# Kernel optimization log

Hardware: AMD Instinct MI355X
Metric: run time of the kernel (lower is better)

## Reference

```python
import jax, jax.numpy as jnp
import numpy as np

B, D, U = 8192, 2048, 2048  # batch rows, input dim, units
NB_FACTOR = 3
MASK_DENSITY = 1.0 / 16.0  # butterfly-like sparse factor density


def _glorot_uniform(key, shape):
    fan_in, fan_out = shape[0], shape[-1]
    limit = np.sqrt(6.0 / (fan_in + fan_out)).astype(np.float32)
    return jax.random.uniform(key, shape, jnp.float32, -limit, limit)


def setup_inputs() -> dict:
    key = jax.random.key(0)
    kx, km0, km1, km2, kk0, kk1, kk2, ks = jax.random.split(key, 8)
    x = jax.random.normal(kx, (B, D), jnp.float32)
    # Fixed sparsity patterns (constants, like K.constant sparsity_masks)
    m0 = (jax.random.uniform(km0, (D, U)) < MASK_DENSITY).astype(jnp.float32)
    m1 = (jax.random.uniform(km1, (U, U)) < MASK_DENSITY).astype(jnp.float32)
    m2 = (jax.random.uniform(km2, (U, U)) < MASK_DENSITY).astype(jnp.float32)
    k0 = _glorot_uniform(kk0, (D, U))
    k1 = _glorot_uniform(kk1, (U, U))
    k2 = _glorot_uniform(kk2, (U, U))
    scaling = _glorot_uniform(ks, (1,))  # scaler weight, shape (1,)
    bias = jnp.zeros((U,), jnp.float32)
    return {"x": x, "k0": k0, "k1": k1, "k2": k2,
            "m0": m0, "m1": m1, "m2": m2,
            "scaling": scaling, "bias": bias}


def reference(x, k0, k1, k2, m0, m1, m2, scaling, bias):
    # output = activation(scaling * (x @ (k0*m0) @ (k1*m1) @ (k2*m2)) + bias)
    out = x @ (k0 * m0)          # [B, U]
    out = out @ (k1 * m1)        # [B, U]
    out = out @ (k2 * m2)        # [B, U]
    out = scaling * out + bias   # scale then channels-last bias add
    return jax.nn.relu(out)
```

## Files before the change

### kernel.cpp

```cpp
#include <hip/hip_runtime.h>
#include <hip/hip_bf16.h>


typedef __attribute__((ext_vector_type(8))) short  short8;
typedef __attribute__((ext_vector_type(8))) ushort ushort8v;
typedef __attribute__((ext_vector_type(4))) float  f32x4;

#define KD 2048
#define ND 2048

__device__ __forceinline__ ushort f2b(float f) {
    union { float f; unsigned u; } v; v.f = f;
    unsigned r = v.u + 0x7fffu + ((v.u >> 16) & 1u);
    return (ushort)(r >> 16);
}

__device__ __forceinline__ void gload16(const ushort* g, ushort* l) {
    __builtin_amdgcn_global_load_lds(
        (const __attribute__((address_space(1))) void*)g,
        (__attribute__((address_space(3))) void*)l, 16, 0, 0);
}

__global__ __launch_bounds__(256)
void convx(const float* __restrict__ x, ushort* __restrict__ xb)
{
    const size_t i = (size_t)blockIdx.x * 256 + threadIdx.x;
    const float4* src = reinterpret_cast<const float4*>(x) + i * 2;
    const float4 f0 = src[0], f1 = src[1];
    ushort8v u;
    u[0]=f2b(f0.x); u[1]=f2b(f0.y); u[2]=f2b(f0.z); u[3]=f2b(f0.w);
    u[4]=f2b(f1.x); u[5]=f2b(f1.y); u[6]=f2b(f1.z); u[7]=f2b(f1.w);
    reinterpret_cast<ushort8v*>(xb)[i] = u;
}

__global__ __launch_bounds__(256)
void convT3(const float* __restrict__ k0w, const float* __restrict__ k1w,
            const float* __restrict__ k2w, const float* __restrict__ m0w,
            const float* __restrict__ m1w, const float* __restrict__ m2w,
            ushort* __restrict__ wbT)
{
    const int z = blockIdx.z;
    const float* kw = z == 0 ? k0w : (z == 1 ? k1w : k2w);
    const float* mw = z == 0 ? m0w : (z == 1 ? m1w : m2w);
    ushort* o = wbT + (size_t)z * KD * ND;

    __shared__ ushort t[32][36];
    const int tid = threadIdx.x;
    const int bk = blockIdx.x * 32, bn = blockIdx.y * 32;
    {
        const int r = tid >> 3, c = (tid & 7) * 4;
        const size_t g = (size_t)(bk + r) * ND + bn + c;
        const float4 kv = *reinterpret_cast<const float4*>(kw + g);
        const float4 mv = *reinterpret_cast<const float4*>(mw + g);
        t[r][c + 0] = f2b(kv.x * mv.x);
        t[r][c + 1] = f2b(kv.y * mv.y);
        t[r][c + 2] = f2b(kv.z * mv.z);
        t[r][c + 3] = f2b(kv.w * mv.w);
    }
    __syncthreads();
    {
        const int n = tid >> 3, kq = (tid & 7) * 4;
        ushort4 ov;
        ov.x = t[kq + 0][n]; ov.y = t[kq + 1][n];
        ov.z = t[kq + 2][n]; ov.w = t[kq + 3][n];
        *reinterpret_cast<ushort4*>(&o[(size_t)(bn + n) * KD + bk + kq]) = ov;
    }
}

template<int EPI>
__global__ __launch_bounds__(512, 2)
void gemm256(const ushort* __restrict__ A, const ushort* __restrict__ BT,
             void* __restrict__ Cout,
             const float* __restrict__ scaling, const float* __restrict__ bias)
{
    __shared__ ushort S[2][2][2][256 * 32];

    const int tid  = threadIdx.x;
    const int lane = tid & 63;
    const int wid  = tid >> 6;
    const int wr   = wid >> 2, wc = wid & 3;
    const int l15  = lane & 15;
    const int kq   = lane >> 4;
    const int id   = blockIdx.x;
    const int swz  = (id & 7) * 32 + (id >> 3);
    const int bn   = (swz & 7) * 256;
    const int bm   = (swz >> 3) * 256;
    const int srow = lane >> 2;
    const int wrow = wid * 32;
    const int ssw  = ((lane & 3) ^ ((srow >> 1) & 3)) * 8;
    const int rsw  = (kq ^ ((l15 >> 1) & 3)) * 8;

    f32x4 acc[8][4] = {};
    short8 xa0, xa1, xa2, xa3, xa4, xa5, xa6, xa7, ya0, ya1, ya2, ya3;

#define STAGE(op, bufl, kh, tile, G, g0) do {                                        \
    gload16(G + (size_t)((g0) + wrow + srow)      * KD + (tile)*64 + (kh)*32 + ssw,  \
            &S[bufl][op][kh][(wrow)      * 32]);                                     \
    gload16(G + (size_t)((g0) + wrow + 16 + srow) * KD + (tile)*64 + (kh)*32 + ssw,  \
            &S[bufl][op][kh][(wrow + 16) * 32]);                                     \
  } while (0)

#define BAR()  asm volatile("s_barrier" ::: "memory")
#define VM0()  asm volatile("s_waitcnt vmcnt(0)" ::: "memory")
#define LGK0() asm volatile("s_waitcnt lgkmcnt(0)" ::: "memory")
#define SB()   __builtin_amdgcn_sched_barrier(0)
#define PRI1() __builtin_amdgcn_s_setprio(1)
#define PRI0() __builtin_amdgcn_s_setprio(0)

#define FA(bufl, kh, m) (*(const short8*)&S[bufl][0][kh][(wr*128 + (m)*16 + l15)*32 + rsw])
#define FB(bufl, kh, n) (*(const short8*)&S[bufl][1][kh][(wc*64  + (n)*16 + l15)*32 + rsw])

#define MF(a_, b_, c_) __builtin_amdgcn_mfma_f32_16x16x32_bf16(a_, b_, c_, 0, 0, 0)

#define READS(bufl, kh)                                                               \
    ya0 = FB(bufl,kh,0); ya1 = FB(bufl,kh,1);                                         \
    ya2 = FB(bufl,kh,2); ya3 = FB(bufl,kh,3);                                         \
    xa0 = FA(bufl,kh,0); xa1 = FA(bufl,kh,1);                                         \
    xa2 = FA(bufl,kh,2); xa3 = FA(bufl,kh,3);                                         \
    xa4 = FA(bufl,kh,4); xa5 = FA(bufl,kh,5);                                         \
    xa6 = FA(bufl,kh,6); xa7 = FA(bufl,kh,7);

#define MMROW(m, xm)                                                                  \
    acc[m][0] = MF(ya0, xm, acc[m][0]);                                               \
    acc[m][1] = MF(ya1, xm, acc[m][1]);                                               \
    acc[m][2] = MF(ya2, xm, acc[m][2]);                                               \
    acc[m][3] = MF(ya3, xm, acc[m][3]);

#define MMALL()                                                                       \
    MMROW(0, xa0) MMROW(1, xa1) MMROW(2, xa2) MMROW(3, xa3)                           \
    MMROW(4, xa4) MMROW(5, xa5) MMROW(6, xa6) MMROW(7, xa7)

#define INTERVAL(bufl, STG1, STG2, GATE) do {                                         \
    STG1;                                                                             \
    READS(bufl, 0);                                                                   \
    PRI1(); MMALL(); PRI0();                                                          \
    STG2;                                                                             \
    READS(bufl, 1);                                                                   \
    PRI1(); MMALL(); PRI0(); SB();                                                    \
    LGK0(); GATE; BAR();                                                              \
  } while (0)

    STAGE(0, 0, 0, 0, A,  bm); STAGE(1, 0, 0, 0, BT, bn);
    STAGE(0, 0, 1, 0, A,  bm); STAGE(1, 0, 1, 0, BT, bn);
    VM0();
    BAR();

    for (int t = 0; t < 31; ++t) {
        const int bf = t & 1;
        INTERVAL(bf,
                 STAGE(0, bf ^ 1, 0, t + 1, A, bm); STAGE(1, bf ^ 1, 0, t + 1, BT, bn),
                 STAGE(0, bf ^ 1, 1, t + 1, A, bm); STAGE(1, bf ^ 1, 1, t + 1, BT, bn),
                 VM0());
    }
    READS(1, 0);
    PRI1(); MMALL(); PRI0();
    READS(1, 1);
    PRI1(); MMALL(); PRI0();

    const float sc = EPI ? scaling[0] : 0.f;
#pragma unroll
    for (int m = 0; m < 8; ++m) {
        const size_t grow = (size_t)(bm + wr * 128 + m * 16 + l15);
#pragma unroll
        for (int n = 0; n < 4; ++n) {
            const int gcol = bn + wc * 64 + n * 16 + kq * 4;
            if constexpr (EPI) {
                const float4 bv = *reinterpret_cast<const float4*>(bias + gcol);
                float4 v;
                v.x = fmaxf(fmaf(sc, acc[m][n][0], bv.x), 0.f);
                v.y = fmaxf(fmaf(sc, acc[m][n][1], bv.y), 0.f);
                v.z = fmaxf(fmaf(sc, acc[m][n][2], bv.z), 0.f);
                v.w = fmaxf(fmaf(sc, acc[m][n][3], bv.w), 0.f);
                *reinterpret_cast<float4*>((float*)Cout + grow * ND + gcol) = v;
            } else {
                ushort4 v;
                v.x = f2b(acc[m][n][0]); v.y = f2b(acc[m][n][1]);
                v.z = f2b(acc[m][n][2]); v.w = f2b(acc[m][n][3]);
                *reinterpret_cast<ushort4*>((ushort*)Cout + grow * ND + gcol) = v;
            }
        }
    }
#undef STAGE
#undef INTERVAL
#undef MF
#undef MMROW
#undef MMALL
#undef READS
#undef FA
#undef FB
}

extern "C" void kernel_launch(void* const* d_in, const int* in_sizes, int n_in,
                              void* d_out, int out_size, void* d_ws, size_t ws_size,
                              hipStream_t stream)
{
    const float* x    = (const float*)d_in[0];
    const float* k0w  = (const float*)d_in[1];
    const float* k1w  = (const float*)d_in[2];
    const float* k2w  = (const float*)d_in[3];
    const float* m0w  = (const float*)d_in[4];
    const float* m1w  = (const float*)d_in[5];
    const float* m2w  = (const float*)d_in[6];
    const float* sc   = (const float*)d_in[7];
    const float* bias = (const float*)d_in[8];

    const int Md = in_sizes[0] / KD;
    const size_t NE = (size_t)Md * KD;

    ushort* act1 = (ushort*)d_out;
    ushort* xb   = (ushort*)d_out + NE;
    float*  out  = (float*)d_out;
    ushort* act2 = (ushort*)d_ws;
    ushort* wbT  = (ushort*)d_ws + NE;

    dim3 bl(256);
    dim3 gX(NE / (256 * 8));
    dim3 gT(KD / 32, ND / 32, 3);
    dim3 gG((ND / 256) * (Md / 256)), bG(512);

    convx <<<gX, bl, 0, stream>>>(x, xb);
    convT3<<<gT, bl, 0, stream>>>(k0w, k1w, k2w, m0w, m1w, m2w, wbT);

    gemm256<0><<<gG, bG, 0, stream>>>(xb,   wbT,                     act1, nullptr, nullptr);
    gemm256<0><<<gG, bG, 0, stream>>>(act1, wbT + (size_t)KD * ND,     act2, nullptr, nullptr);
    gemm256<1><<<gG, bG, 0, stream>>>(act2, wbT + (size_t)2 * KD * ND, out,  sc, bias);
}
```

Baseline: 218.9 us.

## Load B operand fragments directly from global into registers, bypassing LDS

The B (weight) tile is no longer staged through shared memory. Each wave now loads its own B MFMA fragments directly from global memory into registers, double-buffered across k-halves, while A stays staged in LDS. This halves LDS footprint and LDS read traffic per tile and aims to raise occupancy. The cost is that B fragments are re-fetched from global or cache by each of the two row-waves, with less coalesced 16-byte loads, and the loads are exposed to global latency inside the compute loop.

```diff
diff --git a/kernel.cpp b/kernel.cpp
--- a/kernel.cpp
+++ b/kernel.cpp
@@ -73,7 +73,7 @@
              void* __restrict__ Cout,
              const float* __restrict__ scaling, const float* __restrict__ bias)
 {
-    __shared__ ushort S[2][2][2][256 * 32];
+    __shared__ ushort S[2][2][256 * 32];
 
     const int tid  = threadIdx.x;
     const int lane = tid & 63;
@@ -90,72 +90,74 @@
     const int ssw  = ((lane & 3) ^ ((srow >> 1) & 3)) * 8;
     const int rsw  = (kq ^ ((l15 >> 1) & 3)) * 8;
 
+    const ushort* Bb = BT + (size_t)(bn + wc * 64 + l15) * KD + kq * 8;
+
     f32x4 acc[8][4] = {};
-    short8 xa0, xa1, xa2, xa3, xa4, xa5, xa6, xa7, ya0, ya1, ya2, ya3;
-
-#define STAGE(op, bufl, kh, tile, G, g0) do {                                        \
-    gload16(G + (size_t)((g0) + wrow + srow)      * KD + (tile)*64 + (kh)*32 + ssw,  \
-            &S[bufl][op][kh][(wrow)      * 32]);                                     \
-    gload16(G + (size_t)((g0) + wrow + 16 + srow) * KD + (tile)*64 + (kh)*32 + ssw,  \
-            &S[bufl][op][kh][(wrow + 16) * 32]);                                     \
+    short8 xa0, xa1, xa2, xa3, xa4, xa5, xa6, xa7;
+    short8 yb0, yb1, yb2, yb3;
+    short8 zb0, zb1, zb2, zb3;
+
+#define STAGE_A(bufl, kh, tile) do {                                                 \
+    gload16(A + (size_t)(bm + wrow + srow)      * KD + (tile)*64 + (kh)*32 + ssw,    \
+            &S[bufl][kh][(wrow)      * 32]);                                         \
+    gload16(A + (size_t)(bm + wrow + 16 + srow) * KD + (tile)*64 + (kh)*32 + ssw,    \
+            &S[bufl][kh][(wrow + 16) * 32]);                                         \
   } while (0)
 
 #define BAR()  asm volatile("s_barrier" ::: "memory")
 #define VM0()  asm volatile("s_waitcnt vmcnt(0)" ::: "memory")
 #define LGK0() asm volatile("s_waitcnt lgkmcnt(0)" ::: "memory")
-#define SB()   __builtin_amdgcn_sched_barrier(0)
 #define PRI1() __builtin_amdgcn_s_setprio(1)
 #define PRI0() __builtin_amdgcn_s_setprio(0)
 
-#define FA(bufl, kh, m) (*(const short8*)&S[bufl][0][kh][(wr*128 + (m)*16 + l15)*32 + rsw])
-#define FB(bufl, kh, n) (*(const short8*)&S[bufl][1][kh][(wc*64  + (n)*16 + l15)*32 + rsw])
-
-#define MF(a_, b_, c_) __builtin_amdgcn_mfma_f32_16x16x32_bf16(a_, b_, c_, 0, 0, 0)
-
-#define READS(bufl, kh)                                                               \
-    ya0 = FB(bufl,kh,0); ya1 = FB(bufl,kh,1);                                         \
-    ya2 = FB(bufl,kh,2); ya3 = FB(bufl,kh,3);                                         \
+#define FA(bufl, kh, m) (*(const short8*)&S[bufl][kh][(wr*128 + (m)*16 + l15)*32 + rsw])
+
+#define LDB(dst, n, t, kh)                                                            \
+    dst = *reinterpret_cast<const short8*>(Bb + (size_t)(n) * 16 * KD + (t)*64 + (kh)*32);
+
+#define READSA(bufl, kh)                                                              \
     xa0 = FA(bufl,kh,0); xa1 = FA(bufl,kh,1);                                         \
     xa2 = FA(bufl,kh,2); xa3 = FA(bufl,kh,3);                                         \
     xa4 = FA(bufl,kh,4); xa5 = FA(bufl,kh,5);                                         \
     xa6 = FA(bufl,kh,6); xa7 = FA(bufl,kh,7);
 
-#define MMROW(m, xm)                                                                  \
-    acc[m][0] = MF(ya0, xm, acc[m][0]);                                               \
-    acc[m][1] = MF(ya1, xm, acc[m][1]);                                               \
-    acc[m][2] = MF(ya2, xm, acc[m][2]);                                               \
-    acc[m][3] = MF(ya3, xm, acc[m][3]);
-
-#define MMALL()                                                                       \
-    MMROW(0, xa0) MMROW(1, xa1) MMROW(2, xa2) MMROW(3, xa3)                           \
-    MMROW(4, xa4) MMROW(5, xa5) MMROW(6, xa6) MMROW(7, xa7)
-
-#define INTERVAL(bufl, STG1, STG2, GATE) do {                                         \
-    STG1;                                                                             \
-    READS(bufl, 0);                                                                   \
-    PRI1(); MMALL(); PRI0();                                                          \
-    STG2;                                                                             \
-    READS(bufl, 1);                                                                   \
-    PRI1(); MMALL(); PRI0(); SB();                                                    \
-    LGK0(); GATE; BAR();                                                              \
-  } while (0)
-
-    STAGE(0, 0, 0, 0, A,  bm); STAGE(1, 0, 0, 0, BT, bn);
-    STAGE(0, 0, 1, 0, A,  bm); STAGE(1, 0, 1, 0, BT, bn);
+#define MF(a_, b_, c_) __builtin_amdgcn_mfma_f32_16x16x32_bf16(a_, b_, c_, 0, 0, 0)
+
+#define MMROW(m, xm, B0, B1, B2, B3)                                                  \
+    acc[m][0] = MF(B0, xm, acc[m][0]);                                                \
+    acc[m][1] = MF(B1, xm, acc[m][1]);                                                \
+    acc[m][2] = MF(B2, xm, acc[m][2]);                                                \
+    acc[m][3] = MF(B3, xm, acc[m][3]);
+
+#define MMALL(B0, B1, B2, B3)                                                         \
+    MMROW(0, xa0, B0, B1, B2, B3) MMROW(1, xa1, B0, B1, B2, B3)                       \
+    MMROW(2, xa2, B0, B1, B2, B3) MMROW(3, xa3, B0, B1, B2, B3)                       \
+    MMROW(4, xa4, B0, B1, B2, B3) MMROW(5, xa5, B0, B1, B2, B3)                       \
+    MMROW(6, xa6, B0, B1, B2, B3) MMROW(7, xa7, B0, B1, B2, B3)
+
+    STAGE_A(0, 0, 0); STAGE_A(0, 1, 0);
+    LDB(yb0, 0, 0, 0); LDB(yb1, 1, 0, 0); LDB(yb2, 2, 0, 0); LDB(yb3, 3, 0, 0);
     VM0();
     BAR();
 
     for (int t = 0; t < 31; ++t) {
         const int bf = t & 1;
-        INTERVAL(bf,
-                 STAGE(0, bf ^ 1, 0, t + 1, A, bm); STAGE(1, bf ^ 1, 0, t + 1, BT, bn),
-                 STAGE(0, bf ^ 1, 1, t + 1, A, bm); STAGE(1, bf ^ 1, 1, t + 1, BT, bn),
-                 VM0());
-    }
-    READS(1, 0);
-    PRI1(); MMALL(); PRI0();
-    READS(1, 1);
-    PRI1(); MMALL(); PRI0();
+        READSA(bf, 0);
+        LDB(zb0, 0, t, 1); LDB(zb1, 1, t, 1); LDB(zb2, 2, t, 1); LDB(zb3, 3, t, 1);
+        STAGE_A(bf ^ 1, 0, t + 1);
+        PRI1(); MMALL(yb0, yb1, yb2, yb3); PRI0();
+        READSA(bf, 1);
+        LDB(yb0, 0, t + 1, 0); LDB(yb1, 1, t + 1, 0);
+        LDB(yb2, 2, t + 1, 0); LDB(yb3, 3, t + 1, 0);
+        STAGE_A(bf ^ 1, 1, t + 1);
+        PRI1(); MMALL(zb0, zb1, zb2, zb3); PRI0();
+        LGK0(); VM0(); BAR();
+    }
+    READSA(1, 0);
+    LDB(zb0, 0, 31, 1); LDB(zb1, 1, 31, 1); LDB(zb2, 2, 31, 1); LDB(zb3, 3, 31, 1);
+    PRI1(); MMALL(yb0, yb1, yb2, yb3); PRI0();
+    READSA(1, 1);
+    PRI1(); MMALL(zb0, zb1, zb2, zb3); PRI0();
 
     const float sc = EPI ? scaling[0] : 0.f;
 #pragma unroll
@@ -180,14 +182,13 @@
             }
         }
     }
-#undef STAGE
-#undef INTERVAL
+#undef STAGE_A
 #undef MF
 #undef MMROW
 #undef MMALL
-#undef READS
+#undef READSA
+#undef LDB
 #undef FA
-#undef FB
 }
 
 extern "C" void kernel_launch(void* const* d_in, const int* in_sizes, int n_in,
```

After: 303.9 us. +38.8%, slower.
